# Performance work log

Hardware: AMD Instinct MI355X
Metric: run time of the kernel (lower is better)

Reference implementation:

```python
import jax, jax.numpy as jnp
import numpy as np

N_NODES = 100000
N_EDGES = 1600000
IN_DIM, HID_DIM, OUT_DIM = 128, 256, 128


def setup_inputs() -> dict:
    key = jax.random.key(0)
    ks = jax.random.split(key, 5)
    x = jax.random.normal(ks[0], (N_NODES, IN_DIM), dtype=jnp.float32)
    src = jax.random.randint(ks[1], (N_EDGES,), 0, N_NODES, dtype=jnp.int64)
    dst = jax.random.randint(ks[2], (N_EDGES,), 0, N_NODES, dtype=jnp.int64)
    # Glorot-ish init for linear weights (DGL GraphConv default), zero bias
    W1 = jax.random.normal(ks[3], (IN_DIM, HID_DIM), dtype=jnp.float32) * (1.0 / np.sqrt(IN_DIM))
    W2 = jax.random.normal(ks[4], (HID_DIM, OUT_DIM), dtype=jnp.float32) * (1.0 / np.sqrt(HID_DIM))
    b1 = jnp.zeros((HID_DIM,), dtype=jnp.float32)
    b2 = jnp.zeros((OUT_DIM,), dtype=jnp.float32)
    return {"x": x, "src": src, "dst": dst, "W1": W1, "b1": b1, "W2": W2, "b2": b2}


def _degree_norms(src, dst, n_nodes):
    # norm='both': D_out(src)^{-1/2} on messages, D_in(dst)^{-1/2} on aggregate;
    # degrees clamped to min 1 as in DGL.
    ones = jnp.ones(src.shape[0], dtype=jnp.float32)
    deg_out = jax.ops.segment_sum(ones, src, num_segments=n_nodes)
    deg_in = jax.ops.segment_sum(ones, dst, num_segments=n_nodes)
    norm_src = jax.lax.rsqrt(jnp.maximum(deg_out, 1.0))
    norm_dst = jax.lax.rsqrt(jnp.maximum(deg_in, 1.0))
    return norm_src, norm_dst


def _graph_conv(x, src, dst, W, b, norm_src, norm_dst):
    h = x * norm_src[:, None]                                  # [N, d]
    agg = jax.ops.segment_sum(h[src], dst, num_segments=x.shape[0])  # [N, d]
    agg = agg * norm_dst[:, None]
    return agg @ W + b


def reference(x, src, dst, W1, b1, W2, b2):
    norm_src, norm_dst = _degree_norms(src, dst, x.shape[0])
    h = jax.nn.relu(_graph_conv(x, src, dst, W1, b1, norm_src, norm_dst))
    out = _graph_conv(h, src, dst, W2, b2, norm_src, norm_dst)
    return out
```

## Files before the change

kernel.cpp:

```cpp
#include <hip/hip_runtime.h>

constexpr int N_NODES = 100000;
constexpr int N_EDGES = 1600000;
constexpr int DIN = 128, DHID = 256, DOUT = 128;

constexpr int NB = 256;
constexpr int BR = 391;
constexpr int CAP = 8192;
constexpr int NBLK1 = 256;
constexpr int CHUNK = (N_EDGES + NBLK1 - 1) / NBLK1;
constexpr int NIT = (CHUNK + 511) / 512;

typedef __bf16 bf16x8 __attribute__((ext_vector_type(8)));
typedef float f32x4 __attribute__((ext_vector_type(4)));

static __device__ __forceinline__ ushort f2bf(float f) {
    uint u = __float_as_uint(f);
    uint r = (u + 0x7FFFu + ((u >> 16) & 1u)) >> 16;
    return (ushort)r;
}
static __device__ __forceinline__ float bf2f(ushort h) {
    return __uint_as_float(((uint)h) << 16);
}
static __device__ __forceinline__ float bflo(uint w) { return __uint_as_float(w << 16); }
static __device__ __forceinline__ float bfhi(uint w) { return __uint_as_float(w & 0xFFFF0000u); }

__global__ __launch_bounds__(512) void part_kernel(const int* __restrict__ src,
                                                   const int* __restrict__ dst,
                                                   int* __restrict__ curA, int* __restrict__ curB,
                                                   uint* __restrict__ ppair,
                                                   ushort* __restrict__ psv, int e,
                                                   const float* __restrict__ W1,
                                                   ushort* __restrict__ Wf1,
                                                   const float* __restrict__ W2,
                                                   ushort* __restrict__ Wf2) {
    const int t = threadIdx.x;
    if (blockIdx.x >= NBLK1) {
        int i = (blockIdx.x - NBLK1) * 512 + t;
        if (i < DIN * DHID) {
            int frag = i >> 9, r = i & 511;
            int lane = r >> 3, ee = r & 7;
            int kb = frag & 3, ii = (frag >> 2) & 1, w = (frag >> 3) & 3, kh = frag >> 5;
            int c = w * 32 + ii * 16 + (lane & 15);
            int k = kb * 32 + (lane >> 4) * 8 + ee;
            Wf1[i] = f2bf(W1[k * DHID + kh * 128 + c]);
        } else {
            int i2 = i - DIN * DHID;
            int frag = i2 >> 9, r = i2 & 511;
            int lane = r >> 3, ee = r & 7;
            int kb2 = frag & 3, j2 = (frag >> 2) & 1, w = (frag >> 3) & 3, kh = frag >> 5;
            int c2 = w * 32 + j2 * 16 + (lane & 15);
            int k2 = kh * 128 + kb2 * 32 + (lane >> 4) * 8 + ee;
            Wf2[i2] = f2bf(W2[k2 * DOUT + c2]);
        }
        return;
    }
    __shared__ int hA[NB], hB[NB], rA[NB], rB[NB], cA[NB], cB[NB];
    const int b0 = blockIdx.x * CHUNK;
    const int cnt = min(e - b0, CHUNK);
    if (t < NB) { hA[t] = 0; hB[t] = 0; cA[t] = 0; cB[t] = 0; }
    __syncthreads();

    int sA[NIT], dA[NIT];
#pragma unroll
    for (int i = 0; i < NIT; i++) {
        int idx = i * 512 + t;
        if (idx < cnt) {
            sA[i] = src[b0 + idx];
            dA[i] = dst[b0 + idx];
            atomicAdd(&hA[dA[i] / BR], 1);
            atomicAdd(&hB[sA[i] / BR], 1);
        }
    }
    __syncthreads();
    if (t < NB) {
        rA[t] = atomicAdd(&curA[t], hA[t]);
        rB[t] = atomicAdd(&curB[t], hB[t]);
    }
    __syncthreads();
#pragma unroll
    for (int i = 0; i < NIT; i++) {
        int idx = i * 512 + t;
        if (idx < cnt) {
            int s = sA[i], d = dA[i];
            int bd = d / BR;
            int bs = s / BR;
            int p = rA[bd] + atomicAdd(&cA[bd], 1);
            if (p < CAP) ppair[(size_t)bd * CAP + p] = ((uint)(d - bd * BR) << 17) | (uint)s;
            int q = rB[bs] + atomicAdd(&cB[bs], 1);
            if (q < CAP) psv[(size_t)bs * CAP + q] = (ushort)(s - bs * BR);
        }
    }
}

__global__ __launch_bounds__(512) void csrn_kernel(const int* __restrict__ curA,
                                                   const int* __restrict__ curB,
                                                   const uint* __restrict__ ppair,
                                                   const ushort* __restrict__ psv,
                                                   int* __restrict__ csr,
                                                   int* __restrict__ rowstart,
                                                   float* __restrict__ ndst,
                                                   float* __restrict__ nsrc,
                                                   const float* __restrict__ x,
                                                   ushort* __restrict__ xb, int n, int e) {
    __shared__ uint ploc[CAP];
    __shared__ int hist[512], sc[512], exc[512], cur[512];
    __shared__ int sbst;
    const int t = threadIdx.x;
    const int b = blockIdx.x & 255;
    const int side = blockIdx.x >> 8;
    const int first = b * BR;
    const int nr = min(BR, n - first);
    const size_t base = (size_t)b * CAP;

    if (side == 0) {
        const int cntA = min(curA[b], CAP);
        if (t < 256) sc[t] = curA[t];
        __syncthreads();
        for (int off = 1; off < 256; off <<= 1) {
            int add = 0;
            if (t < 256 && t >= off) add = sc[t - off];
            __syncthreads();
            if (t < 256) sc[t] += add;
            __syncthreads();
        }
        if (t == 0) {
            sbst = (b == 0) ? 0 : sc[b - 1];
            if (b == 0) rowstart[n] = e;
        }
        hist[t] = 0;
        cur[t] = 0;
        __syncthreads();
        const int bst = sbst;

        for (int i = t; i < cntA; i += 512) {
            uint p = ppair[base + i];
            ploc[i] = p;
            atomicAdd(&hist[p >> 17], 1);
        }
        __syncthreads();
        int h = hist[t];
        sc[t] = h;
        __syncthreads();
        for (int off = 1; off < 512; off <<= 1) {
            int add = (t >= off) ? sc[t - off] : 0;
            __syncthreads();
            sc[t] += add;
            __syncthreads();
        }
        exc[t] = sc[t] - h;
        if (t < nr) {
            rowstart[first + t] = bst + exc[t];
            ndst[first + t] = rsqrtf(fmaxf((float)h, 1.0f));
        }
        __syncthreads();
        for (int i = t; i < cntA; i += 512) {
            uint p = ploc[i];
            int dl = p >> 17;
            int pos = exc[dl] + atomicAdd(&cur[dl], 1);
            csr[bst + pos] = (int)(p & 0x1FFFFu);
        }
    } else {
        if (nr <= 0) return;
        hist[t] = 0;
        __syncthreads();
        const int cntB = min(curB[b], CAP);
        for (int i = t; i < cntB; i += 512) atomicAdd(&hist[psv[base + i]], 1);
        __syncthreads();
        float* nsv = (float*)exc;
        if (t < nr) {
            float v = rsqrtf(fmaxf((float)hist[t], 1.0f));
            nsrc[first + t] = v;
            nsv[t] = v;
        }
        __syncthreads();
        const int rl = t >> 5, q = t & 31;
        for (int i = rl; i < nr; i += 16) {
            float s = nsv[i];
            const size_t ro = (size_t)(first + i) * 128;
            float4 v = *(const float4*)&x[ro + q * 4];
            ushort4 o = {f2bf(v.x * s), f2bf(v.y * s), f2bf(v.z * s), f2bf(v.w * s)};
            *(ushort4*)&xb[ro + q * 4] = o;
        }
    }
}

template <bool OUTBF16, bool ADDBIAS>
__global__ __launch_bounds__(256) void aggh_kernel(const ushort* __restrict__ Xb,
                                                   const int* __restrict__ csr,
                                                   const int* __restrict__ rowstart,
                                                   const float* __restrict__ ndst,
                                                   const float* __restrict__ bias,
                                                   float* __restrict__ outf,
                                                   ushort* __restrict__ outb, int n, int G) {
    const int half = (blockIdx.x >= G) ? 1 : 0;
    const int bid = blockIdx.x - half * G;
    int g = threadIdx.x >> 3;
    int lane = threadIdx.x & 7;
    int d = bid * 32 + g;
    if (d >= n) return;
    int beg = rowstart[d], end = rowstart[d + 1];
    const int fo = half * 64 + lane * 8;
    const ushort* Xp = Xb + fo;
    float acc[8];
#pragma unroll
    for (int j = 0; j < 8; j++) acc[j] = 0.f;

#define ACC8(v)                                   \
    do {                                          \
        acc[0] += bflo(v.x); acc[1] += bfhi(v.x); \
        acc[2] += bflo(v.y); acc[3] += bfhi(v.y); \
        acc[4] += bflo(v.z); acc[5] += bfhi(v.z); \
        acc[6] += bflo(v.w); acc[7] += bfhi(v.w); \
    } while (0)

    int k = beg;
    for (; k + 8 <= end; k += 8) {
        int s0 = csr[k], s1 = csr[k + 1], s2 = csr[k + 2], s3 = csr[k + 3];
        int s4 = csr[k + 4], s5 = csr[k + 5], s6 = csr[k + 6], s7 = csr[k + 7];
        uint4 v0 = *(const uint4*)(Xp + (size_t)s0 * 128);
        uint4 v1 = *(const uint4*)(Xp + (size_t)s1 * 128);
        uint4 v2 = *(const uint4*)(Xp + (size_t)s2 * 128);
        uint4 v3 = *(const uint4*)(Xp + (size_t)s3 * 128);
        uint4 v4 = *(const uint4*)(Xp + (size_t)s4 * 128);
        uint4 v5 = *(const uint4*)(Xp + (size_t)s5 * 128);
        uint4 v6 = *(const uint4*)(Xp + (size_t)s6 * 128);
        uint4 v7 = *(const uint4*)(Xp + (size_t)s7 * 128);
        ACC8(v0);
        ACC8(v1);
        ACC8(v2);
        ACC8(v3);
        ACC8(v4);
        ACC8(v5);
        ACC8(v6);
        ACC8(v7);
    }
    for (; k + 4 <= end; k += 4) {
        int s0 = csr[k], s1 = csr[k + 1], s2 = csr[k + 2], s3 = csr[k + 3];
        uint4 v0 = *(const uint4*)(Xp + (size_t)s0 * 128);
        uint4 v1 = *(const uint4*)(Xp + (size_t)s1 * 128);
        uint4 v2 = *(const uint4*)(Xp + (size_t)s2 * 128);
        uint4 v3 = *(const uint4*)(Xp + (size_t)s3 * 128);
        ACC8(v0);
        ACC8(v1);
        ACC8(v2);
        ACC8(v3);
    }
    for (; k < end; ++k) {
        uint4 v = *(const uint4*)(Xp + (size_t)csr[k] * 128);
        ACC8(v);
    }
#undef ACC8

    float nd = ndst[d];
#pragma unroll
    for (int j = 0; j < 8; j++) acc[j] *= nd;
    if constexpr (ADDBIAS) {
        float4 b0 = *(const float4*)&bias[fo];
        float4 b1 = *(const float4*)&bias[fo + 4];
        acc[0] += b0.x; acc[1] += b0.y; acc[2] += b0.z; acc[3] += b0.w;
        acc[4] += b1.x; acc[5] += b1.y; acc[6] += b1.z; acc[7] += b1.w;
    }
    if constexpr (OUTBF16) {
        uint4 o;
        o.x = (uint)f2bf(acc[0]) | ((uint)f2bf(acc[1]) << 16);
        o.y = (uint)f2bf(acc[2]) | ((uint)f2bf(acc[3]) << 16);
        o.z = (uint)f2bf(acc[4]) | ((uint)f2bf(acc[5]) << 16);
        o.w = (uint)f2bf(acc[6]) | ((uint)f2bf(acc[7]) << 16);
        *(uint4*)(outb + (size_t)d * 128 + fo) = o;
    } else {
        float4 o0 = {acc[0], acc[1], acc[2], acc[3]};
        float4 o1 = {acc[4], acc[5], acc[6], acc[7]};
        *(float4*)(outf + (size_t)d * 128 + fo) = o0;
        *(float4*)(outf + (size_t)d * 128 + fo + 4) = o1;
    }
}

__global__ __launch_bounds__(256) void fused64_kernel(const ushort* __restrict__ A,
                                                      const ushort* __restrict__ Wf1,
                                                      const float* __restrict__ b1,
                                                      const float* __restrict__ nsrc,
                                                      const ushort* __restrict__ Wf2,
                                                      ushort* __restrict__ T, int M) {
    __shared__ ushort Sa[64][128];
    __shared__ ushort H1[64][128];
    const int row0 = blockIdx.x * 64;
    const int t = threadIdx.x;
    const int w = t >> 6, lane = t & 63;
    const int l16 = lane & 15, lk = lane >> 4;

    float nsv[4];
#pragma unroll
    for (int j = 0; j < 4; j++) {
        int gm = row0 + j * 16 + l16;
        nsv[j] = nsrc[gm < M ? gm : (M - 1)];
    }
    float4 bvv[2][2];
#pragma unroll
    for (int kh = 0; kh < 2; kh++)
#pragma unroll
        for (int i = 0; i < 2; i++)
            bvv[kh][i] = *(const float4*)&b1[kh * 128 + w * 32 + i * 16 + lk * 4];

#pragma unroll
    for (int i = 0; i < 4; i++) {
        int idx = i * 256 + t;
        int r = idx >> 4, oct = idx & 15;
        int gr = row0 + r;
        uint4 v = make_uint4(0u, 0u, 0u, 0u);
        if (gr < M) v = *(const uint4*)&A[(size_t)gr * 128 + oct * 8];
        *(uint4*)((char*)&Sa[0][0] + r * 256 + (oct ^ (r & 15)) * 16) = v;
    }
    __syncthreads();

    f32x4 acc2[4][2];
#pragma unroll
    for (int i = 0; i < 4; i++)
#pragma unroll
        for (int j = 0; j < 2; j++) acc2[i][j] = (f32x4){0.f, 0.f, 0.f, 0.f};

    for (int kh = 0; kh < 2; kh++) {
        const ushort* w1p = Wf1 + ((size_t)(kh * 4 + w) * 8) * 512 + lane * 8;
        const ushort* w2p = Wf2 + ((size_t)(kh * 4 + w) * 8) * 512 + lane * 8;
        bf16x8 af[2][4], wb[2][4];
#pragma unroll
        for (int i = 0; i < 2; i++)
#pragma unroll
            for (int kb = 0; kb < 4; kb++) af[i][kb] = *(const bf16x8*)(w1p + (i * 4 + kb) * 512);
#pragma unroll
        for (int j2 = 0; j2 < 2; j2++)
#pragma unroll
            for (int kb2 = 0; kb2 < 4; kb2++)
                wb[j2][kb2] = *(const bf16x8*)(w2p + (j2 * 4 + kb2) * 512);

        f32x4 acc1[2][4];
#pragma unroll
        for (int i = 0; i < 2; i++)
#pragma unroll
            for (int j = 0; j < 4; j++) acc1[i][j] = (f32x4){0.f, 0.f, 0.f, 0.f};

#pragma unroll
        for (int kb = 0; kb < 4; kb++) {
            bf16x8 bf_[4];
#pragma unroll
            for (int j = 0; j < 4; j++) {
                int m = j * 16 + l16;
                bf_[j] = *(const bf16x8*)((const char*)&Sa[0][0] + m * 256 +
                                          ((kb * 4 + lk) ^ l16) * 16);
            }
#pragma unroll
            for (int i = 0; i < 2; i++)
#pragma unroll
                for (int j = 0; j < 4; j++)
                    acc1[i][j] =
                        __builtin_amdgcn_mfma_f32_16x16x32_bf16(af[i][kb], bf_[j], acc1[i][j], 0, 0, 0);
        }
        __syncthreads();

#pragma unroll
        for (int i = 0; i < 2; i++) {
            int cb = w * 32 + i * 16 + lk * 4;
            float4 bv = bvv[kh][i];
#pragma unroll
            for (int j = 0; j < 4; j++) {
                int m = j * 16 + l16;
                float ns = nsv[j];
                ushort4 pk;
                pk.x = f2bf(fmaxf(acc1[i][j][0] + bv.x, 0.f) * ns);
                pk.y = f2bf(fmaxf(acc1[i][j][1] + bv.y, 0.f) * ns);
                pk.z = f2bf(fmaxf(acc1[i][j][2] + bv.z, 0.f) * ns);
                pk.w = f2bf(fmaxf(acc1[i][j][3] + bv.w, 0.f) * ns);
                int oct = cb >> 3;
                *(ushort4*)((char*)&H1[0][0] + m * 256 + ((oct ^ l16) & 15) * 16 +
                            (cb & 7) * 2) = pk;
            }
        }
        __syncthreads();

#pragma unroll
        for (int kb2 = 0; kb2 < 4; kb2++) {
            bf16x8 ha[4];
#pragma unroll
            for (int i2 = 0; i2 < 4; i2++) {
                int m = i2 * 16 + l16;
                ha[i2] = *(const bf16x8*)((const char*)&H1[0][0] + m * 256 +
                                          ((kb2 * 4 + lk) ^ l16) * 16);
            }
#pragma unroll
            for (int i2 = 0; i2 < 4; i2++)
#pragma unroll
                for (int j2 = 0; j2 < 2; j2++)
                    acc2[i2][j2] = __builtin_amdgcn_mfma_f32_16x16x32_bf16(ha[i2], wb[j2][kb2],
                                                                           acc2[i2][j2], 0, 0, 0);
        }
    }

#pragma unroll
    for (int i2 = 0; i2 < 4; i2++) {
#pragma unroll
        for (int j2 = 0; j2 < 2; j2++) {
#pragma unroll
            for (int q = 0; q < 4; q++) {
                int r = row0 + i2 * 16 + lk * 4 + q;
                int c = w * 32 + j2 * 16 + l16;
                if (r < M) T[(size_t)r * DOUT + c] = f2bf(acc2[i2][j2][q]);
            }
        }
    }
}

extern "C" void kernel_launch(void* const* d_in, const int* in_sizes, int n_in,
                              void* d_out, int out_size, void* d_ws, size_t ws_size,
                              hipStream_t stream) {
    const float* x  = (const float*)d_in[0];
    const int*   src = (const int*)d_in[1];
    const int*   dst = (const int*)d_in[2];
    const float* W1 = (const float*)d_in[3];
    const float* b1 = (const float*)d_in[4];
    const float* W2 = (const float*)d_in[5];
    const float* b2 = (const float*)d_in[6];
    float* out = (float*)d_out;

    const int N = N_NODES, E = N_EDGES;

    size_t off = 0;
    auto carve = [&](size_t bytes) -> void* {
        void* p = (char*)d_ws + off;
        off += (bytes + 255) & ~(size_t)255;
        return p;
    };
    int* curA     = (int*)carve(NB * 4);
    int* curB     = (int*)carve(NB * 4);
    int* rowstart = (int*)carve((size_t)(N + 1) * 4);
    float* ndst   = (float*)carve((size_t)N * 4);
    float* nsrc   = (float*)carve((size_t)N * 4);
    int* csr      = (int*)carve((size_t)E * 4);
    ushort* Wf1   = (ushort*)carve(DIN * DHID * 2);
    ushort* Wf2   = (ushort*)carve(DHID * DOUT * 2);
    ushort* xb    = (ushort*)carve((size_t)N * DIN * 2);
    ushort* agg1b = (ushort*)carve((size_t)N * DIN * 2);
    ushort* tb    = (ushort*)carve((size_t)N * DOUT * 2);
    uint*   ppair = (uint*)carve((size_t)NB * CAP * 4);
    ushort* psv   = (ushort*)carve((size_t)NB * CAP * 2);

    hipMemsetAsync(curA, 0, 2 * NB * 4, stream);

    part_kernel<<<NBLK1 + 128, 512, 0, stream>>>(src, dst, curA, curB, ppair, psv, E,
                                                 W1, Wf1, W2, Wf2);
    csrn_kernel<<<2 * NB, 512, 0, stream>>>(curA, curB, ppair, psv, csr, rowstart, ndst, nsrc,
                                            x, xb, N, E);

    const int gagg = (N + 31) / 32;
    aggh_kernel<true, false><<<2 * gagg, 256, 0, stream>>>(xb, csr, rowstart, ndst, nullptr,
                                                           nullptr, agg1b, N, gagg);

    fused64_kernel<<<(N + 63) / 64, 256, 0, stream>>>(agg1b, Wf1, b1, nsrc, Wf2, tb, N);

    aggh_kernel<false, true><<<2 * gagg, 256, 0, stream>>>(tb, csr, rowstart, ndst, b2,
                                                           out, nullptr, N, gagg);
}
```

Baseline: 197.5 us.

## Fuse first-layer neighbor aggregation into the fused GEMM kernel

The first-layer gather-sum over CSR neighbors now runs inside the fused two-GEMM kernel, which writes the normalized aggregate straight into shared memory instead of round-tripping it through a global bf16 buffer. This drops one kernel launch and the write and re-read of the N x 128 intermediate. In exchange, the gather runs with 64-row blocks and 16 threads per row, a different parallel layout than the dedicated aggregation kernel. That layout may cut occupancy or latency hiding during the irregular gathers, and the GEMM phase now waits on gather latency.

```diff
diff --git a/kernel.cpp b/kernel.cpp
--- a/kernel.cpp
+++ b/kernel.cpp
@@ -276,12 +276,15 @@
     }
 }
 
-__global__ __launch_bounds__(256) void fused64_kernel(const ushort* __restrict__ A,
-                                                      const ushort* __restrict__ Wf1,
-                                                      const float* __restrict__ b1,
-                                                      const float* __restrict__ nsrc,
-                                                      const ushort* __restrict__ Wf2,
-                                                      ushort* __restrict__ T, int M) {
+__global__ __launch_bounds__(256) void gfused_kernel(const ushort* __restrict__ Xb,
+                                                     const int* __restrict__ csr,
+                                                     const int* __restrict__ rowstart,
+                                                     const float* __restrict__ ndst,
+                                                     const ushort* __restrict__ Wf1,
+                                                     const float* __restrict__ b1,
+                                                     const float* __restrict__ nsrc,
+                                                     const ushort* __restrict__ Wf2,
+                                                     ushort* __restrict__ T, int M) {
     __shared__ ushort Sa[64][128];
     __shared__ ushort H1[64][128];
     const int row0 = blockIdx.x * 64;
@@ -302,14 +305,54 @@
         for (int i = 0; i < 2; i++)
             bvv[kh][i] = *(const float4*)&b1[kh * 128 + w * 32 + i * 16 + lk * 4];
 
-#pragma unroll
-    for (int i = 0; i < 4; i++) {
-        int idx = i * 256 + t;
-        int r = idx >> 4, oct = idx & 15;
-        int gr = row0 + r;
-        uint4 v = make_uint4(0u, 0u, 0u, 0u);
-        if (gr < M) v = *(const uint4*)&A[(size_t)gr * 128 + oct * 8];
-        *(uint4*)((char*)&Sa[0][0] + r * 256 + (oct ^ (r & 15)) * 16) = v;
+    {
+        const int grp = t >> 4;
+        const int gl = t & 15;
+        const ushort* Xp = Xb + gl * 8;
+#pragma unroll
+        for (int rep = 0; rep < 4; rep++) {
+            int m = rep * 16 + grp;
+            int d = row0 + m;
+            float acc[8];
+#pragma unroll
+            for (int j = 0; j < 8; j++) acc[j] = 0.f;
+            if (d < M) {
+                int beg = rowstart[d], end = rowstart[d + 1];
+#define ACC8(v)                                   \
+    do {                                          \
+        acc[0] += bflo(v.x); acc[1] += bfhi(v.x); \
+        acc[2] += bflo(v.y); acc[3] += bfhi(v.y); \
+        acc[4] += bflo(v.z); acc[5] += bfhi(v.z); \
+        acc[6] += bflo(v.w); acc[7] += bfhi(v.w); \
+    } while (0)
+                int k = beg;
+                for (; k + 4 <= end; k += 4) {
+                    int s0 = csr[k], s1 = csr[k + 1], s2 = csr[k + 2], s3 = csr[k + 3];
+                    uint4 v0 = *(const uint4*)(Xp + (size_t)s0 * 128);
+                    uint4 v1 = *(const uint4*)(Xp + (size_t)s1 * 128);
+                    uint4 v2 = *(const uint4*)(Xp + (size_t)s2 * 128);
+                    uint4 v3 = *(const uint4*)(Xp + (size_t)s3 * 128);
+                    ACC8(v0);
+                    ACC8(v1);
+                    ACC8(v2);
+                    ACC8(v3);
+                }
+                for (; k < end; ++k) {
+                    uint4 v = *(const uint4*)(Xp + (size_t)csr[k] * 128);
+                    ACC8(v);
+                }
+#undef ACC8
+                float nd = ndst[d];
+#pragma unroll
+                for (int j = 0; j < 8; j++) acc[j] *= nd;
+            }
+            uint4 o;
+            o.x = (uint)f2bf(acc[0]) | ((uint)f2bf(acc[1]) << 16);
+            o.y = (uint)f2bf(acc[2]) | ((uint)f2bf(acc[3]) << 16);
+            o.z = (uint)f2bf(acc[4]) | ((uint)f2bf(acc[5]) << 16);
+            o.w = (uint)f2bf(acc[6]) | ((uint)f2bf(acc[7]) << 16);
+            *(uint4*)((char*)&Sa[0][0] + m * 256 + ((gl ^ (m & 15)) * 16)) = o;
+        }
     }
     __syncthreads();
 
@@ -438,7 +481,6 @@
     ushort* Wf1   = (ushort*)carve(DIN * DHID * 2);
     ushort* Wf2   = (ushort*)carve(DHID * DOUT * 2);
     ushort* xb    = (ushort*)carve((size_t)N * DIN * 2);
-    ushort* agg1b = (ushort*)carve((size_t)N * DIN * 2);
     ushort* tb    = (ushort*)carve((size_t)N * DOUT * 2);
     uint*   ppair = (uint*)carve((size_t)NB * CAP * 4);
     ushort* psv   = (ushort*)carve((size_t)NB * CAP * 2);
@@ -450,12 +492,10 @@
     csrn_kernel<<<2 * NB, 512, 0, stream>>>(curA, curB, ppair, psv, csr, rowstart, ndst, nsrc,
                                             x, xb, N, E);
 
+    gfused_kernel<<<(N + 63) / 64, 256, 0, stream>>>(xb, csr, rowstart, ndst, Wf1, b1, nsrc,
+                                                     Wf2, tb, N);
+
     const int gagg = (N + 31) / 32;
-    aggh_kernel<true, false><<<2 * gagg, 256, 0, stream>>>(xb, csr, rowstart, ndst, nullptr,
-                                                           nullptr, agg1b, N, gagg);
-
-    fused64_kernel<<<(N + 63) / 64, 256, 0, stream>>>(agg1b, Wf1, b1, nsrc, Wf2, tb, N);
-
     aggh_kernel<false, true><<<2 * gagg, 256, 0, stream>>>(tb, csr, rowstart, ndst, b2,
                                                            out, nullptr, N, gagg);
 }
```

Result: slower. 214.8 us (+8.7%).

## Bucket CSR neighbors by source slice to improve gather locality

Applied to the files above, without the earlier changes.

The CSR build now splits each destination row's neighbors into four buckets by source-node range and records per-row slice start offsets. The aggregation kernel walks the four slices in turn, so gathers across concurrently running rows tend to hit the same quarter of the feature table, which is meant to improve L2 hit rates. The cost is extra LDS histograms, a per-node slice offset array, and shorter inner loops that lose the 8-wide unroll and add loop overhead per slice.

```diff
diff --git a/kernel.cpp b/kernel.cpp
--- a/kernel.cpp
+++ b/kernel.cpp
@@ -10,6 +10,8 @@
 constexpr int NBLK1 = 256;
 constexpr int CHUNK = (N_EDGES + NBLK1 - 1) / NBLK1;
 constexpr int NIT = (CHUNK + 511) / 512;
+constexpr int NSL = 4;
+constexpr int SLW = (N_NODES + NSL - 1) / NSL;
 
 typedef __bf16 bf16x8 __attribute__((ext_vector_type(8)));
 typedef float f32x4 __attribute__((ext_vector_type(4)));
@@ -99,12 +101,15 @@
                                                    const ushort* __restrict__ psv,
                                                    int* __restrict__ csr,
                                                    int* __restrict__ rowstart,
+                                                   int* __restrict__ slicestart,
                                                    float* __restrict__ ndst,
                                                    float* __restrict__ nsrc,
                                                    const float* __restrict__ x,
                                                    ushort* __restrict__ xb, int n, int e) {
     __shared__ uint ploc[CAP];
-    __shared__ int hist[512], sc[512], exc[512], cur[512];
+    __shared__ int hist2[BR * NSL];
+    __shared__ int cur2[BR * NSL];
+    __shared__ int sc[512], exc[512];
     __shared__ int sbst;
     const int t = threadIdx.x;
     const int b = blockIdx.x & 255;
@@ -128,18 +133,26 @@
             sbst = (b == 0) ? 0 : sc[b - 1];
             if (b == 0) rowstart[n] = e;
         }
-        hist[t] = 0;
-        cur[t] = 0;
+        for (int i = t; i < BR * NSL; i += 512) {
+            hist2[i] = 0;
+            cur2[i] = 0;
+        }
         __syncthreads();
         const int bst = sbst;
 
         for (int i = t; i < cntA; i += 512) {
             uint p = ppair[base + i];
             ploc[i] = p;
-            atomicAdd(&hist[p >> 17], 1);
-        }
-        __syncthreads();
-        int h = hist[t];
+            int dl = p >> 17;
+            int s = (int)(p & 0x1FFFFu);
+            atomicAdd(&hist2[dl * NSL + s / SLW], 1);
+        }
+        __syncthreads();
+        int h = 0;
+        if (t < nr) {
+#pragma unroll
+            for (int p = 0; p < NSL; p++) h += hist2[t * NSL + p];
+        }
         sc[t] = h;
         __syncthreads();
         for (int off = 1; off < 512; off <<= 1) {
@@ -150,26 +163,35 @@
         }
         exc[t] = sc[t] - h;
         if (t < nr) {
-            rowstart[first + t] = bst + exc[t];
+            int run = bst + exc[t];
+            rowstart[first + t] = run;
             ndst[first + t] = rsqrtf(fmaxf((float)h, 1.0f));
+#pragma unroll
+            for (int p = 0; p < NSL; p++) {
+                int tmp = hist2[t * NSL + p];
+                hist2[t * NSL + p] = run;
+                slicestart[(size_t)(first + t) * NSL + p] = run;
+                run += tmp;
+            }
         }
         __syncthreads();
         for (int i = t; i < cntA; i += 512) {
             uint p = ploc[i];
             int dl = p >> 17;
-            int pos = exc[dl] + atomicAdd(&cur[dl], 1);
-            csr[bst + pos] = (int)(p & 0x1FFFFu);
+            int s = (int)(p & 0x1FFFFu);
+            int pos = hist2[dl * NSL + s / SLW] + atomicAdd(&cur2[dl * NSL + s / SLW], 1);
+            csr[pos] = s;
         }
     } else {
         if (nr <= 0) return;
-        hist[t] = 0;
+        hist2[t] = 0;
         __syncthreads();
         const int cntB = min(curB[b], CAP);
-        for (int i = t; i < cntB; i += 512) atomicAdd(&hist[psv[base + i]], 1);
+        for (int i = t; i < cntB; i += 512) atomicAdd(&hist2[psv[base + i]], 1);
         __syncthreads();
         float* nsv = (float*)exc;
         if (t < nr) {
-            float v = rsqrtf(fmaxf((float)hist[t], 1.0f));
+            float v = rsqrtf(fmaxf((float)hist2[t], 1.0f));
             nsrc[first + t] = v;
             nsv[t] = v;
         }
@@ -189,6 +211,7 @@
 __global__ __launch_bounds__(256) void aggh_kernel(const ushort* __restrict__ Xb,
                                                    const int* __restrict__ csr,
                                                    const int* __restrict__ rowstart,
+                                                   const int* __restrict__ slicestart,
                                                    const float* __restrict__ ndst,
                                                    const float* __restrict__ bias,
                                                    float* __restrict__ outf,
@@ -199,7 +222,8 @@
     int lane = threadIdx.x & 7;
     int d = bid * 32 + g;
     if (d >= n) return;
-    int beg = rowstart[d], end = rowstart[d + 1];
+    const int4 s4 = *(const int4*)&slicestart[(size_t)d * NSL];
+    const int e4 = rowstart[d + 1];
     const int fo = half * 64 + lane * 8;
     const ushort* Xp = Xb + fo;
     float acc[8];
@@ -214,42 +238,27 @@
         acc[6] += bflo(v.w); acc[7] += bfhi(v.w); \
     } while (0)
 
-    int k = beg;
-    for (; k + 8 <= end; k += 8) {
-        int s0 = csr[k], s1 = csr[k + 1], s2 = csr[k + 2], s3 = csr[k + 3];
-        int s4 = csr[k + 4], s5 = csr[k + 5], s6 = csr[k + 6], s7 = csr[k + 7];
-        uint4 v0 = *(const uint4*)(Xp + (size_t)s0 * 128);
-        uint4 v1 = *(const uint4*)(Xp + (size_t)s1 * 128);
-        uint4 v2 = *(const uint4*)(Xp + (size_t)s2 * 128);
-        uint4 v3 = *(const uint4*)(Xp + (size_t)s3 * 128);
-        uint4 v4 = *(const uint4*)(Xp + (size_t)s4 * 128);
-        uint4 v5 = *(const uint4*)(Xp + (size_t)s5 * 128);
-        uint4 v6 = *(const uint4*)(Xp + (size_t)s6 * 128);
-        uint4 v7 = *(const uint4*)(Xp + (size_t)s7 * 128);
-        ACC8(v0);
-        ACC8(v1);
-        ACC8(v2);
-        ACC8(v3);
-        ACC8(v4);
-        ACC8(v5);
-        ACC8(v6);
-        ACC8(v7);
-    }
-    for (; k + 4 <= end; k += 4) {
-        int s0 = csr[k], s1 = csr[k + 1], s2 = csr[k + 2], s3 = csr[k + 3];
-        uint4 v0 = *(const uint4*)(Xp + (size_t)s0 * 128);
-        uint4 v1 = *(const uint4*)(Xp + (size_t)s1 * 128);
-        uint4 v2 = *(const uint4*)(Xp + (size_t)s2 * 128);
-        uint4 v3 = *(const uint4*)(Xp + (size_t)s3 * 128);
-        ACC8(v0);
-        ACC8(v1);
-        ACC8(v2);
-        ACC8(v3);
-    }
-    for (; k < end; ++k) {
-        uint4 v = *(const uint4*)(Xp + (size_t)csr[k] * 128);
-        ACC8(v);
-    }
+    auto seg = [&](int k, int kend) {
+        for (; k + 4 <= kend; k += 4) {
+            int s0 = csr[k], s1 = csr[k + 1], s2 = csr[k + 2], s3 = csr[k + 3];
+            uint4 v0 = *(const uint4*)(Xp + (size_t)s0 * 128);
+            uint4 v1 = *(const uint4*)(Xp + (size_t)s1 * 128);
+            uint4 v2 = *(const uint4*)(Xp + (size_t)s2 * 128);
+            uint4 v3 = *(const uint4*)(Xp + (size_t)s3 * 128);
+            ACC8(v0);
+            ACC8(v1);
+            ACC8(v2);
+            ACC8(v3);
+        }
+        for (; k < kend; ++k) {
+            uint4 v = *(const uint4*)(Xp + (size_t)csr[k] * 128);
+            ACC8(v);
+        }
+    };
+    seg(s4.x, s4.y);
+    seg(s4.y, s4.z);
+    seg(s4.z, s4.w);
+    seg(s4.w, e4);
 #undef ACC8
 
     float nd = ndst[d];
@@ -429,33 +438,34 @@
         off += (bytes + 255) & ~(size_t)255;
         return p;
     };
-    int* curA     = (int*)carve(NB * 4);
-    int* curB     = (int*)carve(NB * 4);
-    int* rowstart = (int*)carve((size_t)(N + 1) * 4);
-    float* ndst   = (float*)carve((size_t)N * 4);
-    float* nsrc   = (float*)carve((size_t)N * 4);
-    int* csr      = (int*)carve((size_t)E * 4);
-    ushort* Wf1   = (ushort*)carve(DIN * DHID * 2);
-    ushort* Wf2   = (ushort*)carve(DHID * DOUT * 2);
-    ushort* xb    = (ushort*)carve((size_t)N * DIN * 2);
-    ushort* agg1b = (ushort*)carve((size_t)N * DIN * 2);
-    ushort* tb    = (ushort*)carve((size_t)N * DOUT * 2);
-    uint*   ppair = (uint*)carve((size_t)NB * CAP * 4);
-    ushort* psv   = (ushort*)carve((size_t)NB * CAP * 2);
+    int* curA       = (int*)carve(NB * 4);
+    int* curB       = (int*)carve(NB * 4);
+    int* rowstart   = (int*)carve((size_t)(N + 1) * 4);
+    int* slicestart = (int*)carve((size_t)N * NSL * 4);
+    float* ndst     = (float*)carve((size_t)N * 4);
+    float* nsrc     = (float*)carve((size_t)N * 4);
+    int* csr        = (int*)carve((size_t)E * 4);
+    ushort* Wf1     = (ushort*)carve(DIN * DHID * 2);
+    ushort* Wf2     = (ushort*)carve(DHID * DOUT * 2);
+    ushort* xb      = (ushort*)carve((size_t)N * DIN * 2);
+    ushort* agg1b   = (ushort*)carve((size_t)N * DIN * 2);
+    ushort* tb      = (ushort*)carve((size_t)N * DOUT * 2);
+    uint*   ppair   = (uint*)carve((size_t)NB * CAP * 4);
+    ushort* psv     = (ushort*)carve((size_t)NB * CAP * 2);
 
     hipMemsetAsync(curA, 0, 2 * NB * 4, stream);
 
     part_kernel<<<NBLK1 + 128, 512, 0, stream>>>(src, dst, curA, curB, ppair, psv, E,
                                                  W1, Wf1, W2, Wf2);
-    csrn_kernel<<<2 * NB, 512, 0, stream>>>(curA, curB, ppair, psv, csr, rowstart, ndst, nsrc,
-                                            x, xb, N, E);
+    csrn_kernel<<<2 * NB, 512, 0, stream>>>(curA, curB, ppair, psv, csr, rowstart, slicestart,
+                                            ndst, nsrc, x, xb, N, E);
 
     const int gagg = (N + 31) / 32;
-    aggh_kernel<true, false><<<2 * gagg, 256, 0, stream>>>(xb, csr, rowstart, ndst, nullptr,
-                                                           nullptr, agg1b, N, gagg);
+    aggh_kernel<true, false><<<2 * gagg, 256, 0, stream>>>(xb, csr, rowstart, slicestart, ndst,
+                                                           nullptr, nullptr, agg1b, N, gagg);
 
     fused64_kernel<<<(N + 63) / 64, 256, 0, stream>>>(agg1b, Wf1, b1, nsrc, Wf2, tb, N);
 
-    aggh_kernel<false, true><<<2 * gagg, 256, 0, stream>>>(tb, csr, rowstart, ndst, b2,
-                                                           out, nullptr, N, gagg);
-}
+    aggh_kernel<false, true><<<2 * gagg, 256, 0, stream>>>(tb, csr, rowstart, slicestart, ndst,
+                                                           b2, out, nullptr, N, gagg);
+}
```

Result: slower. 205.8 us (+4.2%).
